# Kernel optimization log

Hardware: AMD Instinct MI355X
Metric: run time of the kernel (lower is better)

The kernel has to match this reference:

```python
import jax, jax.numpy as jnp
import numpy as np
from jax import lax

B, C, D, H, W = 2, 256, 16, 16, 16
Cq = C // 4


def _conv3d(x, w, b, pad):
    # x: [B,C,D,H,W], w: [O,I,kd,kh,kw]
    y = lax.conv_general_dilated(x, w, (1, 1, 1), pad,
                                 dimension_numbers=("NCDHW", "OIDHW", "NCDHW"))
    return y + b[None, :, None, None, None]


def _ln_ch(x, scale, bias, eps=1e-5):
    # LayerNorm over channel dim (torch normalizes last dim after permute)
    mu = jnp.mean(x, axis=1, keepdims=True)
    var = jnp.var(x, axis=1, keepdims=True)
    y = (x - mu) * lax.rsqrt(var + eps)
    return y * scale[None, :, None, None, None] + bias[None, :, None, None, None]


def setup_inputs() -> dict:
    key = jax.random.key(0)
    ks = jax.random.split(key, 16)
    s = 0.05
    inp = {
        "x": jax.random.normal(ks[0], (B, C, D, H, W), jnp.float32),
        "w1": jax.random.normal(ks[1], (Cq, Cq, 1, 1, 1), jnp.float32) * s,
        "b1": jax.random.normal(ks[2], (Cq,), jnp.float32) * s,
        "w2": jax.random.normal(ks[3], (Cq, Cq, 1, 1, 1), jnp.float32) * s,
        "b2": jax.random.normal(ks[4], (Cq,), jnp.float32) * s,
        "w3": jax.random.normal(ks[5], (Cq, Cq, 1, 1, 1), jnp.float32) * s,
        "b3": jax.random.normal(ks[6], (Cq,), jnp.float32) * s,
        "w4": jax.random.normal(ks[7], (Cq, Cq, 1, 1, 1), jnp.float32) * s,
        "b4": jax.random.normal(ks[8], (Cq,), jnp.float32) * s,
        "wq": jax.random.normal(ks[9], (C, C, 1, 3, 1), jnp.float32) * s,
        "bq": jax.random.normal(ks[10], (C,), jnp.float32) * s,
        "wk": jax.random.normal(ks[11], (C, C, 1, 1, 3), jnp.float32) * s,
        "bk": jax.random.normal(ks[12], (C,), jnp.float32) * s,
        "wv": jax.random.normal(ks[13], (C, C, 3, 1, 1), jnp.float32) * s,
        "bv": jax.random.normal(ks[14], (C,), jnp.float32) * s,
        "q_scale": jnp.ones((C,), jnp.float32),
        "q_bias": jnp.zeros((C,), jnp.float32),
        "k_scale": jnp.ones((C,), jnp.float32),
        "k_bias": jnp.zeros((C,), jnp.float32),
        "v_scale": jnp.ones((C,), jnp.float32),
        "v_bias": jnp.zeros((C,), jnp.float32),
        "gamma": jnp.ones((1,), jnp.float32) * 0.5,
    }
    return inp


def reference(x, w1, b1, w2, b2, w3, b3, w4, b4, wq, bq, wk, bk, wv, bv,
              q_scale, q_bias, k_scale, k_bias, v_scale, v_bias, gamma):
    b, c, d, h, w = x.shape
    n = d * h * w
    p0 = [(0, 0)] * 3
    # channel-split 1x1 convs + SiLU gating (dilation is a no-op for 1x1x1)
    s1 = _conv3d(x[:, 0 * Cq:1 * Cq], w1, b1, p0)
    s2 = _conv3d(x[:, 1 * Cq:2 * Cq], w2, b2, p0)
    s3 = _conv3d(x[:, 2 * Cq:3 * Cq], w3, b3, p0)
    s4 = _conv3d(x[:, 3 * Cq:4 * Cq], w4, b4, p0)
    silu = lambda t: t * jax.nn.sigmoid(t)
    xg = jnp.concatenate([silu(s1), silu(s2), silu(s3), silu(s4)], axis=1)
    # QKV projections with directional kernels + channel LayerNorm
    Q = _ln_ch(_conv3d(xg, wq, bq, [(0, 0), (1, 1), (0, 0)]), q_scale, q_bias)
    K = _ln_ch(_conv3d(xg, wk, bk, [(0, 0), (0, 0), (1, 1)]), k_scale, k_bias)
    V = _ln_ch(_conv3d(xg, wv, bv, [(1, 1), (0, 0), (0, 0)]), v_scale, v_bias)
    Qf = Q.reshape(b, c, n).transpose(0, 2, 1)  # [B, N, C]
    Kf = K.reshape(b, c, n).transpose(0, 2, 1)
    Vf = V.reshape(b, c, n).transpose(0, 2, 1)
    scores = jnp.einsum("bnc,bmc->bnm", Qf, Kf) / (c ** 0.5)  # [B, N, N]
    att = jax.nn.softmax(scores, axis=-1)
    out_a = jnp.einsum("bnm,bmc->bnc", att, Vf)  # [B, N, C]
    out_a = out_a.transpose(0, 2, 1).reshape(b, c, d, h, w)
    return gamma * out_a + xg
```

## Files before the change

### kernel.cpp

```cpp
#include <hip/hip_runtime.h>

#define Bn 2
#define Cn 256
#define Nn 4096
#define SPLIT 4
#define KVB 64
#define NSTEP ((Nn / SPLIT) / KVB)

typedef __attribute__((ext_vector_type(8))) short short8;
typedef __attribute__((ext_vector_type(4))) float f32x4;

__device__ __forceinline__ unsigned short f2bf(float f) {
  union { float f; unsigned int u; } v; v.f = f;
  unsigned int r = (v.u + 0x7FFFu + ((v.u >> 16) & 1u)) >> 16;
  return (unsigned short)r;
}
__device__ __forceinline__ float bf2f(unsigned short u) {
  union { unsigned int i; float f; } v; v.i = ((unsigned int)u) << 16; return v.f;
}

__device__ __forceinline__ f32x4 mfma16(short8 a, short8 b, f32x4 c) {
  return __builtin_amdgcn_mfma_f32_16x16x32_bf16(a, b, c, 0, 0, 0);
}

__global__ __launch_bounds__(256) void gated_prepw_kernel(
    const float* __restrict__ x,
    const float* __restrict__ w1, const float* __restrict__ b1,
    const float* __restrict__ w2, const float* __restrict__ b2,
    const float* __restrict__ w3, const float* __restrict__ b3,
    const float* __restrict__ w4, const float* __restrict__ b4,
    const float* __restrict__ wq, const float* __restrict__ wk,
    const float* __restrict__ wv,
    unsigned short* __restrict__ xgT, unsigned short* __restrict__ w2b) {
  const int bid = blockIdx.x;
  const int tid = threadIdx.x;
  if (bid >= 512) {
    int idx = (bid - 512) * 256 + tid;
    int tensor = idx / 196608;
    int rem = idx % 196608;
    int t  = rem >> 16;
    int co = (rem >> 8) & 255;
    int ci = rem & 255;
    const float* w = (tensor == 0) ? wq : (tensor == 1) ? wk : wv;
    w2b[idx] = f2bf(w[(co * 256 + ci) * 3 + t]);
    return;
  }
  __shared__ float Wl[64][65];
  __shared__ float Xl[64][65];
  __shared__ unsigned short Yl[64][72];
  const int n0 = (bid & 63) * 64;
  const int q  = (bid >> 6) & 3;
  const int b  = bid >> 8;
  const float* wsel = (q == 0) ? w1 : (q == 1) ? w2 : (q == 2) ? w3 : w4;
  const float* bsel = (q == 0) ? b1 : (q == 1) ? b2 : (q == 2) ? b3 : b4;

  #pragma unroll
  for (int it = 0; it < 4; it++) {
    int i = (tid + it * 256) * 4;
    float4 v = *(const float4*)(wsel + i);
    int co = i >> 6, ci = i & 63;
    Wl[co][ci] = v.x; Wl[co][ci + 1] = v.y; Wl[co][ci + 2] = v.z; Wl[co][ci + 3] = v.w;
  }
  {
    int ci = tid >> 2, part = tid & 3;
    const float* src = x + ((size_t)(b * Cn + q * 64 + ci)) * Nn + n0 + part * 16;
    #pragma unroll
    for (int j = 0; j < 4; j++) {
      float4 v = ((const float4*)src)[j];
      float* dst = &Xl[ci][part * 16 + j * 4];
      dst[0] = v.x; dst[1] = v.y; dst[2] = v.z; dst[3] = v.w;
    }
  }
  __syncthreads();
  const int co = tid >> 2, npart = tid & 3;
  float acc[16];
  {
    float bias = bsel[co];
    #pragma unroll
    for (int j = 0; j < 16; j++) acc[j] = bias;
  }
  for (int ci = 0; ci < 64; ci++) {
    float wv_ = Wl[co][ci];
    const float* xr = &Xl[ci][npart * 16];
    #pragma unroll
    for (int j = 0; j < 16; j++) acc[j] += wv_ * xr[j];
  }
  #pragma unroll
  for (int j = 0; j < 16; j++) {
    float v = acc[j];
    float s = v / (1.f + __expf(-v));
    Yl[npart * 16 + j][co] = f2bf(s);
  }
  __syncthreads();
  {
    int r = tid >> 2, cp = tid & 3;
    union { unsigned short u[16]; uint4 v[2]; } pk;
    #pragma unroll
    for (int j = 0; j < 16; j++) pk.u[j] = Yl[r][cp * 16 + j];
    uint4* dst = (uint4*)(xgT + ((size_t)(b * Nn + n0 + r)) * Cn + q * 64 + cp * 16);
    dst[0] = pk.v[0];
    dst[1] = pk.v[1];
  }
}

__global__ __launch_bounds__(128) void qkvconv_ln_kernel(
    const unsigned short* __restrict__ xgT, const unsigned short* __restrict__ w2,
    const float* __restrict__ bq, const float* __restrict__ bk,
    const float* __restrict__ bv,
    const float* __restrict__ qs, const float* __restrict__ qb,
    const float* __restrict__ ks, const float* __restrict__ kb,
    const float* __restrict__ vs, const float* __restrict__ vb,
    unsigned short* __restrict__ qkv) {
  __shared__ unsigned short Al[32 * 72];
  __shared__ unsigned short Bl[256 * 72];
  const int tid = threadIdx.x;
  const int lane = tid & 63, wave = tid >> 6;
  const int l15 = lane & 15, l4 = lane >> 4;
  const int n0  = blockIdx.x * 32;
  const int b = blockIdx.y;
  const int tensor = blockIdx.z;
  const int cstride = (tensor == 0) ? 16 : (tensor == 1) ? 1 : 256;
  const float* bias = (tensor == 0) ? bq : (tensor == 1) ? bk : bv;
  const float* lsc = (tensor == 0) ? qs : (tensor == 1) ? ks : vs;
  const float* lbi = (tensor == 0) ? qb : (tensor == 1) ? kb : vb;
  const unsigned short* wbase = w2 + (size_t)tensor * 196608;
  const unsigned short* xbase = xgT + (size_t)b * Nn * Cn;

  f32x4 acc[16];
  #pragma unroll
  for (int i = 0; i < 16; i++) acc[i] = (f32x4){0.f, 0.f, 0.f, 0.f};

  const int arow = tid >> 2, akp = tid & 3;
  const int n = n0 + arow;
  const int coordv = (n / cstride) & 15;

  for (int kc = 0; kc < 12; kc++) {
    int t = kc >> 2;
    int cib = (kc & 3) * 64;
    int shift = t - 1;
    int c2 = coordv + shift;
    {
      const unsigned short* asrc =
          xbase + ((size_t)(n + shift * cstride)) * Cn + cib + akp * 16;
      uint4 av0 = (c2 >= 0 && c2 < 16) ? ((const uint4*)asrc)[0] : (uint4){0, 0, 0, 0};
      uint4 av1 = (c2 >= 0 && c2 < 16) ? ((const uint4*)asrc)[1] : (uint4){0, 0, 0, 0};
      uint4* ad = (uint4*)(Al + arow * 72 + akp * 16);
      ad[0] = av0; ad[1] = av1;
    }
    {
      #pragma unroll
      for (int i = 0; i < 8; i++) {
        int row = (tid >> 2) + 32 * i;
        const unsigned short* bsrc =
            wbase + ((size_t)(t * 256 + row)) * 256 + cib + akp * 16;
        uint4* bd = (uint4*)(Bl + row * 72 + akp * 16);
        bd[0] = ((const uint4*)bsrc)[0];
        bd[1] = ((const uint4*)bsrc)[1];
      }
    }
    __syncthreads();
    int arowf = wave * 16 + l15;
    #pragma unroll
    for (int kk = 0; kk < 2; kk++) {
      short8 af = *(const short8*)(Al + arowf * 72 + kk * 32 + l4 * 8);
      #pragma unroll
      for (int ct = 0; ct < 16; ct++) {
        int brow = ct * 16 + l15;
        short8 bf = *(const short8*)(Bl + brow * 72 + kk * 32 + l4 * 8);
        acc[ct] = mfma16(af, bf, acc[ct]);
      }
    }
    __syncthreads();
  }

  float bv_[16], scv[16], lbv[16];
  #pragma unroll
  for (int ct = 0; ct < 16; ct++) {
    int c = ct * 16 + l15;
    bv_[ct] = bias[c]; scv[ct] = lsc[c]; lbv[ct] = lbi[c];
  }
  unsigned short* ob = qkv + ((size_t)(tensor * Bn + b) * Nn) * Cn;
  #pragma unroll
  for (int i = 0; i < 4; i++) {
    float s = 0.f, s2 = 0.f;
    #pragma unroll
    for (int ct = 0; ct < 16; ct++) {
      float v = acc[ct][i] + bv_[ct];
      s += v; s2 += v * v;
    }
    s  += __shfl_xor(s, 1);  s  += __shfl_xor(s, 2);
    s  += __shfl_xor(s, 4);  s  += __shfl_xor(s, 8);
    s2 += __shfl_xor(s2, 1); s2 += __shfl_xor(s2, 2);
    s2 += __shfl_xor(s2, 4); s2 += __shfl_xor(s2, 8);
    float mean = s * (1.f / 256.f);
    float var  = s2 * (1.f / 256.f) - mean * mean;
    float inv  = rsqrtf(var + 1e-5f);
    int nn = n0 + wave * 16 + l4 * 4 + i;
    unsigned short* orow = ob + (size_t)nn * Cn;
    #pragma unroll
    for (int ct = 0; ct < 16; ct++) {
      float v = acc[ct][i] + bv_[ct];
      orow[ct * 16 + l15] = f2bf((v - mean) * inv * scv[ct] + lbv[ct]);
    }
  }
}

__global__ __launch_bounds__(256, 2) void flash_kernel(
    const unsigned short* __restrict__ qkv, unsigned short* __restrict__ Opart,
    float* __restrict__ ml) {
  __shared__ unsigned short Ks[KVB][264];
  __shared__ unsigned short Vt[256][72];
  __shared__ unsigned short Pl[4][16][72];
  const int tid = threadIdx.x, lane = tid & 63, wave = tid >> 6;
  const int l15 = lane & 15, l4 = lane >> 4;
  const int qt = blockIdx.x, b = blockIdx.y, sp = blockIdx.z;
  const unsigned short* Q = qkv + (size_t)(0 * Bn + b) * Nn * Cn;
  const unsigned short* K = qkv + (size_t)(1 * Bn + b) * Nn * Cn;
  const unsigned short* V = qkv + (size_t)(2 * Bn + b) * Nn * Cn;
  const int q0 = qt * 64 + wave * 16;

  short8 qf[8];
  {
    const unsigned short* qp = Q + (size_t)(q0 + l15) * Cn + l4 * 8;
    #pragma unroll
    for (int kk = 0; kk < 8; kk++) qf[kk] = *(const short8*)(qp + kk * 32);
  }
  f32x4 acc_o[16];
  #pragma unroll
  for (int i = 0; i < 16; i++) acc_o[i] = (f32x4){0.f, 0.f, 0.f, 0.f};
  float m_r[4], l_r[4];
  #pragma unroll
  for (int i = 0; i < 4; i++) { m_r[i] = -1e30f; l_r[i] = 0.f; }

  const int kvbase = sp * (Nn / SPLIT);
  const float scl = 0.0625f;

  for (int step = 0; step < NSTEP; step++) {
    int kv0 = kvbase + step * KVB;
    {
      int r = tid >> 2, cp = tid & 3;
      const unsigned short* src = K + (size_t)(kv0 + r) * Cn + cp * 64;
      uint4* dst = (uint4*)&Ks[r][cp * 64];
      #pragma unroll
      for (int i = 0; i < 8; i++) dst[i] = ((const uint4*)src)[i];
    }
    {
      int rp = (tid & 31) * 2, ch = (tid >> 5) * 32;
      const unsigned short* s0p = V + (size_t)(kv0 + rp) * Cn + ch;
      const unsigned short* s1p = s0p + Cn;
      union { uint4 v[4]; unsigned short u[32]; } r0, r1;
      #pragma unroll
      for (int i = 0; i < 4; i++) {
        r0.v[i] = ((const uint4*)s0p)[i];
        r1.v[i] = ((const uint4*)s1p)[i];
      }
      #pragma unroll
      for (int j = 0; j < 32; j++) {
        unsigned int pack = (unsigned int)r0.u[j] | ((unsigned int)r1.u[j] << 16);
        *(unsigned int*)&Vt[ch + j][rp] = pack;
      }
    }
    __syncthreads();

    f32x4 s[4];
    #pragma unroll
    for (int t = 0; t < 4; t++) s[t] = (f32x4){0.f, 0.f, 0.f, 0.f};
    #pragma unroll
    for (int kk = 0; kk < 8; kk++) {
      #pragma unroll
      for (int t = 0; t < 4; t++) {
        short8 bt = *(const short8*)&Ks[t * 16 + l15][kk * 32 + l4 * 8];
        s[t] = mfma16(qf[kk], bt, s[t]);
      }
    }

    float p[4][4], al[4];
    #pragma unroll
    for (int i = 0; i < 4; i++) {
      float a0 = s[0][i] * scl, a1 = s[1][i] * scl;
      float a2 = s[2][i] * scl, a3 = s[3][i] * scl;
      float mt = fmaxf(fmaxf(a0, a1), fmaxf(a2, a3));
      mt = fmaxf(mt, __shfl_xor(mt, 1));
      mt = fmaxf(mt, __shfl_xor(mt, 2));
      mt = fmaxf(mt, __shfl_xor(mt, 4));
      mt = fmaxf(mt, __shfl_xor(mt, 8));
      float mn = fmaxf(m_r[i], mt);
      float a = __expf(m_r[i] - mn);
      m_r[i] = mn; al[i] = a;
      p[0][i] = __expf(a0 - mn);
      p[1][i] = __expf(a1 - mn);
      p[2][i] = __expf(a2 - mn);
      p[3][i] = __expf(a3 - mn);
      float r = (p[0][i] + p[1][i]) + (p[2][i] + p[3][i]);
      r += __shfl_xor(r, 1); r += __shfl_xor(r, 2);
      r += __shfl_xor(r, 4); r += __shfl_xor(r, 8);
      l_r[i] = l_r[i] * a + r;
    }
    #pragma unroll
    for (int i = 0; i < 4; i++) {
      int row = l4 * 4 + i;
      #pragma unroll
      for (int t = 0; t < 4; t++)
        Pl[wave][row][t * 16 + l15] = f2bf(p[t][i]);
    }
    #pragma unroll
    for (int ct = 0; ct < 16; ct++)
      #pragma unroll
      for (int i = 0; i < 4; i++) acc_o[ct][i] *= al[i];

    short8 pf0 = *(const short8*)&Pl[wave][l15][l4 * 8];
    short8 pf1 = *(const short8*)&Pl[wave][l15][32 + l4 * 8];
    #pragma unroll
    for (int ct = 0; ct < 16; ct++) {
      short8 vf0 = *(const short8*)&Vt[ct * 16 + l15][l4 * 8];
      short8 vf1 = *(const short8*)&Vt[ct * 16 + l15][32 + l4 * 8];
      acc_o[ct] = mfma16(pf0, vf0, acc_o[ct]);
      acc_o[ct] = mfma16(pf1, vf1, acc_o[ct]);
    }
    __syncthreads();
  }

  unsigned short* ob = Opart + ((size_t)(sp * Bn + b) * Nn) * Cn;
  #pragma unroll
  for (int ct = 0; ct < 16; ct++) {
    int c = ct * 16 + l15;
    #pragma unroll
    for (int i = 0; i < 4; i++) {
      int nn = q0 + l4 * 4 + i;
      ob[(size_t)nn * Cn + c] = f2bf(acc_o[ct][i]);
    }
  }
  if (l15 == 0) {
    #pragma unroll
    for (int i = 0; i < 4; i++) {
      int nn = q0 + l4 * 4 + i;
      size_t mb = (((size_t)sp * Bn + b) * Nn + nn) * 2;
      ml[mb]     = m_r[i];
      ml[mb + 1] = l_r[i];
    }
  }
}

__global__ __launch_bounds__(256) void combine_kernel(
    const unsigned short* __restrict__ Opart, const float* __restrict__ ml,
    const unsigned short* __restrict__ xgT, const float* __restrict__ gamma,
    float* __restrict__ out) {
  __shared__ float T[256][17];
  const int tid = threadIdx.x;
  const int n0 = blockIdx.x * 16;
  const int b = blockIdx.y;
  const float g = gamma[0];
  for (int r = 0; r < 16; r++) {
    int n = n0 + r;
    float msp[SPLIT], lsp[SPLIT];
    float mm = -1e30f;
    #pragma unroll
    for (int s = 0; s < SPLIT; s++) {
      size_t mb = (((size_t)s * Bn + b) * Nn + n) * 2;
      msp[s] = ml[mb]; lsp[s] = ml[mb + 1];
      mm = fmaxf(mm, msp[s]);
    }
    float denom = 0.f, w[SPLIT];
    #pragma unroll
    for (int s = 0; s < SPLIT; s++) { w[s] = __expf(msp[s] - mm); denom += w[s] * lsp[s]; }
    float inv = 1.f / denom;
    float acc = 0.f;
    #pragma unroll
    for (int s = 0; s < SPLIT; s++)
      acc += w[s] * bf2f(Opart[(((size_t)s * Bn + b) * Nn + n) * Cn + tid]);
    float res = bf2f(xgT[((size_t)(b * Nn + n)) * Cn + tid]);
    T[tid][r] = g * acc * inv + res;
  }
  __syncthreads();
  {
    const int cg = tid >> 3;
    const int nl = (tid & 7) * 2;
    #pragma unroll
    for (int j = 0; j < 8; j++) {
      int c = cg + j * 32;
      float2 v;
      v.x = T[c][nl];
      v.y = T[c][nl + 1];
      *(float2*)(out + ((size_t)(b * Cn + c)) * Nn + n0 + nl) = v;
    }
  }
}

extern "C" void kernel_launch(void* const* d_in, const int* in_sizes, int n_in,
                              void* d_out, int out_size, void* d_ws, size_t ws_size,
                              hipStream_t stream) {
  const float* x   = (const float*)d_in[0];
  const float* w1  = (const float*)d_in[1];
  const float* b1  = (const float*)d_in[2];
  const float* w2i = (const float*)d_in[3];
  const float* b2  = (const float*)d_in[4];
  const float* w3  = (const float*)d_in[5];
  const float* b3  = (const float*)d_in[6];
  const float* w4  = (const float*)d_in[7];
  const float* b4  = (const float*)d_in[8];
  const float* wq  = (const float*)d_in[9];
  const float* bq  = (const float*)d_in[10];
  const float* wk  = (const float*)d_in[11];
  const float* bk  = (const float*)d_in[12];
  const float* wv  = (const float*)d_in[13];
  const float* bv  = (const float*)d_in[14];
  const float* qs  = (const float*)d_in[15];
  const float* qb  = (const float*)d_in[16];
  const float* ks  = (const float*)d_in[17];
  const float* kb  = (const float*)d_in[18];
  const float* vs  = (const float*)d_in[19];
  const float* vb  = (const float*)d_in[20];
  const float* gamma = (const float*)d_in[21];
  float* out = (float*)d_out;

  char* ws = (char*)d_ws;
  unsigned short* xgT   = (unsigned short*)(ws + 0);
  unsigned short* w2b   = (unsigned short*)(ws + 4194304);
  unsigned short* qkv   = (unsigned short*)(ws + 5373952);
  unsigned short* Opart = (unsigned short*)(ws + 17956864);
  float* ml             = (float*)(ws + 34734080);

  gated_prepw_kernel<<<dim3(2816), dim3(256), 0, stream>>>(
      x, w1, b1, w2i, b2, w3, b3, w4, b4, wq, wk, wv, xgT, w2b);
  qkvconv_ln_kernel<<<dim3(128, 2, 3), dim3(128), 0, stream>>>(
      xgT, w2b, bq, bk, bv, qs, qb, ks, kb, vs, vb, qkv);
  flash_kernel<<<dim3(64, 2, SPLIT), dim3(256), 0, stream>>>(qkv, Opart, ml);
  combine_kernel<<<dim3(256, 2), dim3(256), 0, stream>>>(Opart, ml, xgT, gamma, out);
}
```

Before: 147.6 us.

## Fuse split-KV combine into flash kernel via last-arriving-block counter

Removes the separate combine kernel launch. Each flash block increments an atomic counter per (query tile, batch) after writing its partial output. The last of the SPLIT blocks then merges the partial results, adds the residual, and writes the transposed output, reusing the K shared buffer as scratch. This saves a launch and the dependency gap between kernels. In exchange it adds a memset and threadfences, and the tail combine work falls on a subset of blocks.

```diff
diff --git a/kernel.cpp b/kernel.cpp
--- a/kernel.cpp
+++ b/kernel.cpp
@@ -207,10 +207,13 @@
 
 __global__ __launch_bounds__(256, 2) void flash_kernel(
     const unsigned short* __restrict__ qkv, unsigned short* __restrict__ Opart,
-    float* __restrict__ ml) {
+    float* __restrict__ ml, const unsigned short* __restrict__ xgT,
+    const float* __restrict__ gamma, float* __restrict__ out,
+    int* __restrict__ cnt) {
   __shared__ unsigned short Ks[KVB][264];
   __shared__ unsigned short Vt[256][72];
   __shared__ unsigned short Pl[4][16][72];
+  __shared__ int sOld;
   const int tid = threadIdx.x, lane = tid & 63, wave = tid >> 6;
   const int l15 = lane & 15, l4 = lane >> 4;
   const int qt = blockIdx.x, b = blockIdx.y, sp = blockIdx.z;
@@ -339,49 +342,52 @@
       ml[mb + 1] = l_r[i];
     }
   }
-}
-
-__global__ __launch_bounds__(256) void combine_kernel(
-    const unsigned short* __restrict__ Opart, const float* __restrict__ ml,
-    const unsigned short* __restrict__ xgT, const float* __restrict__ gamma,
-    float* __restrict__ out) {
-  __shared__ float T[256][17];
-  const int tid = threadIdx.x;
-  const int n0 = blockIdx.x * 16;
-  const int b = blockIdx.y;
-  const float g = gamma[0];
-  for (int r = 0; r < 16; r++) {
-    int n = n0 + r;
-    float msp[SPLIT], lsp[SPLIT];
-    float mm = -1e30f;
-    #pragma unroll
-    for (int s = 0; s < SPLIT; s++) {
-      size_t mb = (((size_t)s * Bn + b) * Nn + n) * 2;
-      msp[s] = ml[mb]; lsp[s] = ml[mb + 1];
-      mm = fmaxf(mm, msp[s]);
-    }
-    float denom = 0.f, w[SPLIT];
-    #pragma unroll
-    for (int s = 0; s < SPLIT; s++) { w[s] = __expf(msp[s] - mm); denom += w[s] * lsp[s]; }
-    float inv = 1.f / denom;
-    float acc = 0.f;
-    #pragma unroll
-    for (int s = 0; s < SPLIT; s++)
-      acc += w[s] * bf2f(Opart[(((size_t)s * Bn + b) * Nn + n) * Cn + tid]);
-    float res = bf2f(xgT[((size_t)(b * Nn + n)) * Cn + tid]);
-    T[tid][r] = g * acc * inv + res;
-  }
+
+  __threadfence();
+  if (tid == 0) sOld = atomicAdd(&cnt[qt * Bn + b], 1);
   __syncthreads();
-  {
-    const int cg = tid >> 3;
-    const int nl = (tid & 7) * 2;
-    #pragma unroll
-    for (int j = 0; j < 8; j++) {
-      int c = cg + j * 32;
-      float2 v;
-      v.x = T[c][nl];
-      v.y = T[c][nl + 1];
-      *(float2*)(out + ((size_t)(b * Cn + c)) * Nn + n0 + nl) = v;
+  if (sOld == SPLIT - 1) {
+    __threadfence();
+    const float g = gamma[0];
+    float* Tl = (float*)&Ks[0][0];
+    #pragma unroll 1
+    for (int sub = 0; sub < 4; sub++) {
+      int nb = qt * 64 + sub * 16;
+      __syncthreads();
+      for (int r = 0; r < 16; r++) {
+        int n = nb + r;
+        float msp[SPLIT], lsp[SPLIT];
+        float mm = -1e30f;
+        #pragma unroll
+        for (int s2 = 0; s2 < SPLIT; s2++) {
+          size_t mb = (((size_t)s2 * Bn + b) * Nn + n) * 2;
+          msp[s2] = ml[mb]; lsp[s2] = ml[mb + 1];
+          mm = fmaxf(mm, msp[s2]);
+        }
+        float denom = 0.f, w[SPLIT];
+        #pragma unroll
+        for (int s2 = 0; s2 < SPLIT; s2++) { w[s2] = __expf(msp[s2] - mm); denom += w[s2] * lsp[s2]; }
+        float inv = 1.f / denom;
+        float acc2 = 0.f;
+        #pragma unroll
+        for (int s2 = 0; s2 < SPLIT; s2++)
+          acc2 += w[s2] * bf2f(Opart[(((size_t)s2 * Bn + b) * Nn + n) * Cn + tid]);
+        float res = bf2f(xgT[((size_t)(b * Nn + n)) * Cn + tid]);
+        Tl[tid * 17 + r] = g * acc2 * inv + res;
+      }
+      __syncthreads();
+      {
+        const int cg = tid >> 3;
+        const int nl = (tid & 7) * 2;
+        #pragma unroll
+        for (int j = 0; j < 8; j++) {
+          int c = cg + j * 32;
+          float2 v;
+          v.x = Tl[c * 17 + nl];
+          v.y = Tl[c * 17 + nl + 1];
+          *(float2*)(out + ((size_t)(b * Cn + c)) * Nn + nb + nl) = v;
+        }
+      }
     }
   }
 }
@@ -419,11 +425,13 @@
   unsigned short* qkv   = (unsigned short*)(ws + 5373952);
   unsigned short* Opart = (unsigned short*)(ws + 17956864);
   float* ml             = (float*)(ws + 34734080);
-
+  int* cnt              = (int*)(ws + 34996224);
+
+  hipMemsetAsync(cnt, 0, 64 * Bn * sizeof(int), stream);
   gated_prepw_kernel<<<dim3(2816), dim3(256), 0, stream>>>(
       x, w1, b1, w2i, b2, w3, b3, w4, b4, wq, wk, wv, xgT, w2b);
   qkvconv_ln_kernel<<<dim3(128, 2, 3), dim3(128), 0, stream>>>(
       xgT, w2b, bq, bk, bv, qs, qb, ks, kb, vs, vb, qkv);
-  flash_kernel<<<dim3(64, 2, SPLIT), dim3(256), 0, stream>>>(qkv, Opart, ml);
-  combine_kernel<<<dim3(256, 2), dim3(256), 0, stream>>>(Opart, ml, xgT, gamma, out);
-}
+  flash_kernel<<<dim3(64, 2, SPLIT), dim3(256), 0, stream>>>(
+      qkv, Opart, ml, xgT, gamma, out, cnt);
+}
```

New measurement: 246.4 us. +66.9%, slower.
